# Optimization experiments

Measured on AMD Instinct MI355X. Metric: run time of the kernel, lower is better.

Reference implementation:

```python
import jax, jax.numpy as jnp
import numpy as np

N_NODES = 100000
N_EDGES = 3200000
HID = 128

def lrelu(x):
    return jax.nn.leaky_relu(x, negative_slope=0.01)

def gcn_conv(x, W, b, src, dst):
    # PyG GCNConv: h = x W; add self-loops; sym-normalized scatter-sum; + bias
    N = x.shape[0]
    h = x @ W                                   # [N, out]
    loop = jnp.arange(N, dtype=src.dtype)
    s = jnp.concatenate([src, loop])
    d = jnp.concatenate([dst, loop])
    deg = jnp.zeros((N,), h.dtype).at[d].add(1.0)
    dinv = jnp.where(deg > 0, jax.lax.rsqrt(deg), 0.0)
    norm = dinv[s] * dinv[d]                    # [E+N]
    msgs = h[s] * norm[:, None]                 # gather + scale
    out = jax.ops.segment_sum(msgs, d, num_segments=N)
    return out + b

def setup_inputs() -> dict:
    key = jax.random.key(0)
    ks = jax.random.split(key, 32)
    f = jnp.float32
    def w(k, shape, fan_in):
        return (jax.random.normal(k, shape, dtype=f) * (1.0 / np.sqrt(fan_in))).astype(f)
    inp = {}
    inp['des'] = jax.random.normal(ks[0], (N_NODES, 768), dtype=f)
    inp['tweet'] = jax.random.normal(ks[1], (N_NODES, 768), dtype=f)
    inp['num_prop'] = jax.random.normal(ks[2], (N_NODES, 5), dtype=f)
    inp['cat_prop'] = jax.random.normal(ks[3], (N_NODES, 1), dtype=f)
    inp['edge_index'] = jax.random.randint(ks[4], (2, N_EDGES), 0, N_NODES, dtype=jnp.int32)
    q = HID // 4
    inp['W_des'] = w(ks[5], (768, q), 768);   inp['b_des'] = jnp.zeros((q,), f)
    inp['W_tweet'] = w(ks[6], (768, q), 768); inp['b_tweet'] = jnp.zeros((q,), f)
    inp['W_num'] = w(ks[7], (5, q), 5);       inp['b_num'] = jnp.zeros((q,), f)
    inp['W_cat'] = w(ks[8], (1, q), 1);       inp['b_cat'] = jnp.zeros((q,), f)
    inp['W_in'] = w(ks[9], (HID, HID), HID);  inp['b_in'] = jnp.zeros((HID,), f)
    inp['W_g1'] = w(ks[10], (HID, HID), HID); inp['b_g1'] = jnp.zeros((HID,), f)
    inp['W_g2'] = w(ks[11], (HID, HID), HID); inp['b_g2'] = jnp.zeros((HID,), f)
    inp['W_o1'] = w(ks[12], (HID, HID), HID); inp['b_o1'] = jnp.zeros((HID,), f)
    inp['W_o2'] = w(ks[13], (HID, 2), HID);   inp['b_o2'] = jnp.zeros((2,), f)
    return inp

def reference(des, tweet, num_prop, cat_prop, edge_index,
              W_des, b_des, W_tweet, b_tweet, W_num, b_num, W_cat, b_cat,
              W_in, b_in, W_g1, b_g1, W_g2, b_g2, W_o1, b_o1, W_o2, b_o2):
    src, dst = edge_index[0], edge_index[1]
    d = lrelu(des @ W_des + b_des)
    t = lrelu(tweet @ W_tweet + b_tweet)
    n = lrelu(num_prop @ W_num + b_num)
    c = lrelu(cat_prop @ W_cat + b_cat)
    x = jnp.concatenate((d, t, n, c), axis=1)   # [N, HID]
    x = lrelu(x @ W_in + b_in)                  # dropout = identity (eval)
    x = gcn_conv(x, W_g1, b_g1, src, dst)
    x = gcn_conv(x, W_g2, b_g2, src, dst)
    x = lrelu(x @ W_o1 + b_o1)
    return x @ W_o2 + b_o2                      # [N, 2]
```

## Files before the change

kernel.cpp:

```cpp
#include <hip/hip_runtime.h>
#include <hip/hip_bf16.h>
#include <cstdint>

#define HID 128
#define BSHIFT 11

typedef short short8 __attribute__((ext_vector_type(8)));
typedef float f32x4 __attribute__((ext_vector_type(4)));

__device__ __forceinline__ unsigned pack_bf16(float a, float b)
{
    __hip_bfloat16 ha = __float2bfloat16(a);
    __hip_bfloat16 hb = __float2bfloat16(b);
    unsigned short ua = *reinterpret_cast<unsigned short*>(&ha);
    unsigned short ub = *reinterpret_cast<unsigned short*>(&hb);
    return (unsigned)ua | ((unsigned)ub << 16);
}

__device__ __forceinline__ float bf16_lo(unsigned u)
{
    unsigned v = u << 16;
    return *reinterpret_cast<float*>(&v);
}
__device__ __forceinline__ float bf16_hi(unsigned u)
{
    unsigned v = u & 0xffff0000u;
    return *reinterpret_cast<float*>(&v);
}

__device__ __forceinline__ void split8(const float* v, short8& h, short8& l)
{
    #pragma unroll
    for (int j = 0; j < 8; ++j) {
        unsigned bits = __float_as_uint(v[j]);
        h[j] = (short)(bits >> 16);
        unsigned hb = bits & 0xffff0000u;
        float lof = v[j] - __uint_as_float(hb);
        l[j] = (short)(__float_as_uint(lof) >> 16);
    }
}

__device__ __forceinline__ short8 frag_ld(const short* __restrict__ base, int tile, int lane)
{
    return *reinterpret_cast<const short8*>(base + (((size_t)tile * 64 + lane) << 3));
}

__device__ __forceinline__ int lds_addr(int row, int unit)
{
    return row * 256 + ((unit ^ (row & 7)) << 4);
}

__global__ void convert_w_kernel(
    const float* W0, const float* W1, const float* W2,
    const float* W3, const float* W4, const float* W5,
    short* H0, short* L0, short* H1, short* L1, short* H2, short* L2,
    short* H3, short* L3, short* H4, short* L4, short* H5, short* L5)
{
    int job = blockIdx.y;
    const float* W; short* H; short* L; int K, C;
    switch (job) {
        case 0: W = W0; H = H0; L = L0; K = 768; C = 32;  break;
        case 1: W = W1; H = H1; L = L1; K = 768; C = 32;  break;
        case 2: W = W2; H = H2; L = L2; K = 128; C = 128; break;
        case 3: W = W3; H = H3; L = L3; K = 128; C = 128; break;
        case 4: W = W4; H = H4; L = L4; K = 128; C = 128; break;
        default: W = W5; H = H5; L = L5; K = 128; C = 128; break;
    }
    int NT = C >> 4;
    int rows = (K >> 5) * NT * 64;
    int r = blockIdx.x * blockDim.x + threadIdx.x;
    if (r >= rows) return;
    int lane = r & 63;
    int tile = r >> 6;
    int c = (tile % NT) * 16 + (lane & 15);
    int kbase = (tile / NT) * 32 + ((lane >> 4) & 3) * 8;
    float v[8];
    #pragma unroll
    for (int j = 0; j < 8; ++j) v[j] = W[(size_t)(kbase + j) * C + c];
    short8 h, l;
    split8(v, h, l);
    *reinterpret_cast<short8*>(H + ((size_t)r << 3)) = h;
    *reinterpret_cast<short8*>(L + ((size_t)r << 3)) = l;
}

__global__ __launch_bounds__(256, 4) void enc_lds_kernel(
    const float* __restrict__ des, const float* __restrict__ tweet,
    const short* __restrict__ wdes_hi, const short* __restrict__ wdes_lo,
    const short* __restrict__ wtw_hi, const short* __restrict__ wtw_lo,
    const float* __restrict__ bd, const float* __restrict__ bt,
    float* __restrict__ x0, int N)
{
    __shared__ char lds[2][16384];
    const int mat = blockIdx.y;
    const float* __restrict__ X = mat ? tweet : des;
    const short* __restrict__ WH = mat ? wtw_hi : wdes_hi;
    const short* __restrict__ WL = mat ? wtw_lo : wdes_lo;
    const float* __restrict__ B = mat ? bt : bd;

    const int t = threadIdx.x;
    const int lane = t & 63;
    const int wv = t >> 6;
    const int n0 = blockIdx.x * 64;

    const int srow_in_seg = lane >> 4;
    const int sunit = lane & 15;

    f32x4 acc0 = {}, acc1 = {};

    auto stage = [&](int b, int p) {
        #pragma unroll
        for (int i = 0; i < 4; ++i) {
            int seg = wv * 4 + i;
            int row = seg * 4 + srow_in_seg;
            int qsrc = sunit ^ (row & 7);
            int rowg = n0 + row;
            if (rowg >= N) rowg = N - 1;
            const char* g = (const char*)X + (size_t)rowg * 3072 + (size_t)p * 256 + qsrc * 16;
            __builtin_amdgcn_global_load_lds((const unsigned*)g,
                                             (unsigned*)&lds[b][seg * 1024], 16, 0, 0);
        }
    };

    const int frow = wv * 16 + (lane & 15);
    const int kq = (lane >> 4) * 2;

    stage(0, 0);
    for (int p = 0; p < 12; ++p) {
        const int b = p & 1;
        if (p < 11) stage(b ^ 1, p + 1);
        __syncthreads();
        #pragma unroll
        for (int kcl = 0; kcl < 2; ++kcl) {
            int q0 = kcl * 8 + kq;
            float4 u0 = *reinterpret_cast<const float4*>(
                &lds[b][frow * 256 + ((q0 ^ (frow & 7)) << 4)]);
            float4 u1 = *reinterpret_cast<const float4*>(
                &lds[b][frow * 256 + (((q0 + 1) ^ (frow & 7)) << 4)]);
            float av[8] = {u0.x, u0.y, u0.z, u0.w, u1.x, u1.y, u1.z, u1.w};
            short8 ah, al;
            split8(av, ah, al);
            int kc = p * 2 + kcl;
            short8 wh0 = frag_ld(WH, kc * 2 + 0, lane);
            short8 wl0 = frag_ld(WL, kc * 2 + 0, lane);
            short8 wh1 = frag_ld(WH, kc * 2 + 1, lane);
            short8 wl1 = frag_ld(WL, kc * 2 + 1, lane);
            acc0 = __builtin_amdgcn_mfma_f32_16x16x32_bf16(ah, wh0, acc0, 0, 0, 0);
            acc1 = __builtin_amdgcn_mfma_f32_16x16x32_bf16(ah, wh1, acc1, 0, 0, 0);
            acc0 = __builtin_amdgcn_mfma_f32_16x16x32_bf16(ah, wl0, acc0, 0, 0, 0);
            acc1 = __builtin_amdgcn_mfma_f32_16x16x32_bf16(ah, wl1, acc1, 0, 0, 0);
            acc0 = __builtin_amdgcn_mfma_f32_16x16x32_bf16(al, wh0, acc0, 0, 0, 0);
            acc1 = __builtin_amdgcn_mfma_f32_16x16x32_bf16(al, wh1, acc1, 0, 0, 0);
        }
        __syncthreads();
    }

    const int cl = lane & 15;
    float b0 = B[cl], b1 = B[16 + cl];
    const int nodeb = n0 + wv * 16 + (lane >> 4) * 4;
    #pragma unroll
    for (int r = 0; r < 4; ++r) {
        int node = nodeb + r;
        if (node < N) {
            float v0 = acc0[r] + b0; v0 = v0 > 0.f ? v0 : 0.01f * v0;
            float v1 = acc1[r] + b1; v1 = v1 > 0.f ? v1 : 0.01f * v1;
            x0[(size_t)node * HID + mat * 32 + cl] = v0;
            x0[(size_t)node * HID + mat * 32 + 16 + cl] = v1;
        }
    }
}

__global__ void enc_nc_kernel(const float* __restrict__ num, const float* __restrict__ cat,
                              const float* __restrict__ Wn, const float* __restrict__ bn,
                              const float* __restrict__ Wc, const float* __restrict__ bc,
                              float* __restrict__ x0, int N)
{
    int tid = blockIdx.x * blockDim.x + threadIdx.x;
    int col = tid & 63;
    int node = tid >> 6;
    if (node >= N) return;
    float a;
    if (col < 32) {
        const float* r = num + (size_t)node * 5;
        float acc = bn[col];
        #pragma unroll
        for (int k = 0; k < 5; ++k) acc = fmaf(r[k], Wn[k * 32 + col], acc);
        a = acc;
    } else {
        int c = col & 31;
        a = fmaf(cat[node], Wc[c], bc[c]);
    }
    a = a > 0.f ? a : 0.01f * a;
    x0[(size_t)node * HID + 64 + col] = a;
}

__global__ __launch_bounds__(512, 4) void fused_x1g1_kernel(
    const float* __restrict__ in,
    const short* __restrict__ WH1, const short* __restrict__ WL1, const float* __restrict__ b1,
    const short* __restrict__ WH2, const short* __restrict__ WL2,
    const float* __restrict__ dinv, unsigned* __restrict__ outp, int N)
{
    __shared__ char lds[8 * 4096];
    const int t = threadIdx.x;
    const int lane = t & 63;
    const int wv = t >> 6;
    const int n0 = blockIdx.x * 128;
    const int arow = n0 + wv * 16 + (lane & 15);
    const bool valid = arow < N;
    const int cl = lane & 15;
    const int rq = lane >> 4;

    f32x4 acc[8] = {};
    #pragma unroll
    for (int kc = 0; kc < 4; ++kc) {
        float av[8] = {};
        if (valid) {
            const float* ap = in + (size_t)arow * HID + rq * 8;
            float4 u0 = *reinterpret_cast<const float4*>(ap + kc * 32);
            float4 u1 = *reinterpret_cast<const float4*>(ap + kc * 32 + 4);
            av[0] = u0.x; av[1] = u0.y; av[2] = u0.z; av[3] = u0.w;
            av[4] = u1.x; av[5] = u1.y; av[6] = u1.z; av[7] = u1.w;
        }
        short8 ah, al;
        split8(av, ah, al);
        #pragma unroll
        for (int nt = 0; nt < 8; ++nt) {
            short8 wh = frag_ld(WH1, kc * 8 + nt, lane);
            short8 wl = frag_ld(WL1, kc * 8 + nt, lane);
            acc[nt] = __builtin_amdgcn_mfma_f32_16x16x32_bf16(ah, wh, acc[nt], 0, 0, 0);
            acc[nt] = __builtin_amdgcn_mfma_f32_16x16x32_bf16(ah, wl, acc[nt], 0, 0, 0);
            acc[nt] = __builtin_amdgcn_mfma_f32_16x16x32_bf16(al, wh, acc[nt], 0, 0, 0);
        }
    }

    char* my = lds + wv * 4096;
    #pragma unroll
    for (int nt = 0; nt < 8; ++nt) {
        float bb = b1[nt * 16 + cl];
        #pragma unroll
        for (int r = 0; r < 4; ++r) {
            float v = acc[nt][r] + bb;
            v = v > 0.f ? v : 0.01f * v;
            float pv = __shfl_xor(v, 1);
            if ((lane & 1) == 0) {
                unsigned uv = pack_bf16(v, pv);
                int row = rq * 4 + r;
                int col = nt * 16 + cl;
                int unit = col >> 3;
                int off = ((col & 7) >> 1) << 2;
                *reinterpret_cast<unsigned*>(my + lds_addr(row, unit) + off) = uv;
            }
        }
    }
    __syncthreads();

    f32x4 acc2[8] = {};
    #pragma unroll
    for (int kc = 0; kc < 4; ++kc) {
        short8 ah = *reinterpret_cast<short8*>(my + lds_addr(cl, kc * 4 + rq));
        #pragma unroll
        for (int nt = 0; nt < 8; ++nt) {
            short8 wh = frag_ld(WH2, kc * 8 + nt, lane);
            short8 wl = frag_ld(WL2, kc * 8 + nt, lane);
            acc2[nt] = __builtin_amdgcn_mfma_f32_16x16x32_bf16(ah, wh, acc2[nt], 0, 0, 0);
            acc2[nt] = __builtin_amdgcn_mfma_f32_16x16x32_bf16(ah, wl, acc2[nt], 0, 0, 0);
        }
    }

    const int nodeb = n0 + wv * 16 + rq * 4;
    float di[4];
    #pragma unroll
    for (int r = 0; r < 4; ++r)
        di[r] = (nodeb + r < N) ? dinv[nodeb + r] : 0.f;
    #pragma unroll
    for (int nt = 0; nt < 8; ++nt) {
        int c = nt * 16 + cl;
        #pragma unroll
        for (int r = 0; r < 4; ++r) {
            float v = acc2[nt][r] * di[r];
            float pv = __shfl_xor(v, 1);
            int node = nodeb + r;
            if ((lane & 1) == 0 && node < N) {
                unsigned u = pack_bf16(v, pv);
                outp[(size_t)node * (HID / 2) + (c >> 1)] = u;
            }
        }
    }
}

template<bool OUT2>
__global__ __launch_bounds__(512, 4) void fused_convgemm_kernel(
    const unsigned* __restrict__ hs, const int* __restrict__ row_ptr,
    const int* __restrict__ col_idx, const float* __restrict__ dinv,
    const float* __restrict__ bconv,
    const short* __restrict__ WH, const short* __restrict__ WL,
    const float* __restrict__ bgem, const float* __restrict__ W2,
    const float* __restrict__ b2, void* __restrict__ outp, int N)
{
    __shared__ char lds[32 * 256];
    __shared__ float red[2][16][4][2];
    const int t = threadIdx.x;
    const int lane = t & 63;
    const int wv = t >> 6;
    const int n0 = blockIdx.x * 32;

    {
        int nl = t >> 4;
        int f = t & 15;
        int node = n0 + nl;
        float a[8] = {};
        if (node < N) {
            const uint4* base = reinterpret_cast<const uint4*>(hs);
            uint4 v0 = base[(size_t)node * 16 + f];
            a[0] = bf16_lo(v0.x); a[1] = bf16_hi(v0.x);
            a[2] = bf16_lo(v0.y); a[3] = bf16_hi(v0.y);
            a[4] = bf16_lo(v0.z); a[5] = bf16_hi(v0.z);
            a[6] = bf16_lo(v0.w); a[7] = bf16_hi(v0.w);
            int e = row_ptr[node], end = row_ptr[node + 1];
            int idx = (e + f < end) ? col_idx[e + f] : 0;
            while (e < end) {
                int m = end - e;
                int curidx = idx;
                if (e + 16 + f < end) idx = col_idx[e + 16 + f];
                if (m >= 16) {
                    #pragma unroll 16
                    for (int j = 0; j < 16; ++j) {
                        int s = __shfl(curidx, j, 16);
                        uint4 v = base[(size_t)s * 16 + f];
                        a[0] += bf16_lo(v.x); a[1] += bf16_hi(v.x);
                        a[2] += bf16_lo(v.y); a[3] += bf16_hi(v.y);
                        a[4] += bf16_lo(v.z); a[5] += bf16_hi(v.z);
                        a[6] += bf16_lo(v.w); a[7] += bf16_hi(v.w);
                    }
                    e += 16;
                } else {
                    for (int j = 0; j < m; ++j) {
                        int s = __shfl(curidx, j, 16);
                        uint4 v = base[(size_t)s * 16 + f];
                        a[0] += bf16_lo(v.x); a[1] += bf16_hi(v.x);
                        a[2] += bf16_lo(v.y); a[3] += bf16_hi(v.y);
                        a[4] += bf16_lo(v.z); a[5] += bf16_hi(v.z);
                        a[6] += bf16_lo(v.w); a[7] += bf16_hi(v.w);
                    }
                    e = end;
                }
            }
            float di = dinv[node];
            const float* bb = bconv + f * 8;
            #pragma unroll
            for (int j = 0; j < 8; ++j) a[j] = fmaf(di, a[j], bb[j]);
        }
        uint4 o;
        o.x = pack_bf16(a[0], a[1]);
        o.y = pack_bf16(a[2], a[3]);
        o.z = pack_bf16(a[4], a[5]);
        o.w = pack_bf16(a[6], a[7]);
        *reinterpret_cast<uint4*>(lds + lds_addr(nl, f)) = o;
    }
    __syncthreads();

    const int cl = lane & 15;
    const int rq = lane >> 4;
    const int mt = wv >> 2;
    const int ntp = wv & 3;
    f32x4 acc[2] = {};
    #pragma unroll
    for (int kc = 0; kc < 4; ++kc) {
        short8 ah = *reinterpret_cast<short8*>(lds + lds_addr(mt * 16 + cl, kc * 4 + rq));
        #pragma unroll
        for (int i = 0; i < 2; ++i) {
            int nt = ntp * 2 + i;
            short8 wh = frag_ld(WH, kc * 8 + nt, lane);
            short8 wl = frag_ld(WL, kc * 8 + nt, lane);
            acc[i] = __builtin_amdgcn_mfma_f32_16x16x32_bf16(ah, wh, acc[i], 0, 0, 0);
            acc[i] = __builtin_amdgcn_mfma_f32_16x16x32_bf16(ah, wl, acc[i], 0, 0, 0);
        }
    }

    const int nodeb = n0 + mt * 16 + rq * 4;

    if (!OUT2) {
        float di[4];
        #pragma unroll
        for (int r = 0; r < 4; ++r)
            di[r] = (nodeb + r < N) ? dinv[nodeb + r] : 0.f;
        #pragma unroll
        for (int i = 0; i < 2; ++i) {
            int c = (ntp * 2 + i) * 16 + cl;
            #pragma unroll
            for (int r = 0; r < 4; ++r) {
                float v = acc[i][r] * di[r];
                float pv = __shfl_xor(v, 1);
                int node = nodeb + r;
                if ((lane & 1) == 0 && node < N) {
                    unsigned u = pack_bf16(v, pv);
                    reinterpret_cast<unsigned*>(outp)[(size_t)node * (HID / 2) + (c >> 1)] = u;
                }
            }
        }
    } else {
        float p0[4] = {}, p1[4] = {};
        #pragma unroll
        for (int i = 0; i < 2; ++i) {
            int c = (ntp * 2 + i) * 16 + cl;
            float bb = bgem[c];
            float w20 = W2[c * 2 + 0], w21 = W2[c * 2 + 1];
            #pragma unroll
            for (int r = 0; r < 4; ++r) {
                float v = acc[i][r] + bb;
                v = v > 0.f ? v : 0.01f * v;
                p0[r] = fmaf(v, w20, p0[r]);
                p1[r] = fmaf(v, w21, p1[r]);
            }
        }
        #pragma unroll
        for (int r = 0; r < 4; ++r) {
            #pragma unroll
            for (int m = 1; m < 16; m <<= 1) {
                p0[r] += __shfl_xor(p0[r], m);
                p1[r] += __shfl_xor(p1[r], m);
            }
        }
        if (cl == 0) {
            #pragma unroll
            for (int r = 0; r < 4; ++r) {
                red[mt][rq * 4 + r][ntp][0] = p0[r];
                red[mt][rq * 4 + r][ntp][1] = p1[r];
            }
        }
        __syncthreads();
        if (t < 64) {
            int nl2 = t >> 1, comp = t & 1;
            int mtt = nl2 >> 4, rr = nl2 & 15;
            float s = red[mtt][rr][0][comp] + red[mtt][rr][1][comp]
                    + red[mtt][rr][2][comp] + red[mtt][rr][3][comp] + b2[comp];
            int node = n0 + nl2;
            if (node < N)
                reinterpret_cast<float*>(outp)[(size_t)node * 2 + comp] = s;
        }
    }
}

__global__ void init_gcur_kernel(int* __restrict__ gcur, int NBUCK, int CAP)
{
    int t = threadIdx.x;
    if (t < NBUCK) gcur[t] = t * CAP;
}

__global__ void partition_kernel(const int* __restrict__ src, const int* __restrict__ dst,
                                 int* __restrict__ gcur, int2* __restrict__ pairs,
                                 int E, int maxpos)
{
    __shared__ int sS[1024], sD[1024];
    __shared__ int bcnt[64], boff[64];
    int nch = (E + 1023) >> 10;
    for (int ch = blockIdx.x; ch < nch; ch += gridDim.x) {
        int base = ch << 10;
        int cnt = E - base; if (cnt > 1024) cnt = 1024;
        for (int i = threadIdx.x; i < cnt; i += 256) { sS[i] = src[base + i]; sD[i] = dst[base + i]; }
        if (threadIdx.x < 64) bcnt[threadIdx.x] = 0;
        __syncthreads();
        for (int i = threadIdx.x; i < cnt; i += 256) atomicAdd(&bcnt[sD[i] >> BSHIFT], 1);
        __syncthreads();
        if (threadIdx.x < 64 && bcnt[threadIdx.x] > 0)
            boff[threadIdx.x] = atomicAdd(&gcur[threadIdx.x], bcnt[threadIdx.x]);
        __syncthreads();
        if (threadIdx.x < 64) bcnt[threadIdx.x] = 0;
        __syncthreads();
        for (int i = threadIdx.x; i < cnt; i += 256) {
            int d = sD[i];
            int b = d >> BSHIFT;
            int r = atomicAdd(&bcnt[b], 1);
            int pos = boff[b] + r;
            if (pos < maxpos) pairs[pos] = make_int2(sS[i], d);
        }
        __syncthreads();
    }
}

__global__ void hist_bucket_kernel(const int2* __restrict__ pairs, const int* __restrict__ gcur,
                                   int* __restrict__ cnt, int CAP, int N)
{
    __shared__ int lc[2048];
    int b = blockIdx.x;
    int half = blockIdx.y;
    int beg = b * CAP;
    int size = gcur[b] - beg;
    for (int i = threadIdx.x; i < 2048; i += 256) lc[i] = 0;
    __syncthreads();
    int s0 = beg + half * (size >> 1);
    int s1 = half ? (beg + size) : (beg + (size >> 1));
    for (int i = s0 + threadIdx.x; i < s1; i += 256)
        atomicAdd(&lc[pairs[i].y & 2047], 1);
    __syncthreads();
    int nodeb = b << BSHIFT;
    for (int i = threadIdx.x; i < 2048; i += 256) {
        if (lc[i] && nodeb + i < N) atomicAdd(&cnt[nodeb + i], lc[i]);
    }
}

__global__ void scan_block_kernel(const int* __restrict__ cnt, int* __restrict__ excl_out,
                                  int* __restrict__ part, int N)
{
    __shared__ int s[256];
    int t = threadIdx.x;
    int i = blockIdx.x * 256 + t;
    int v = (i < N) ? cnt[i] : 0;
    s[t] = v;
    __syncthreads();
    #pragma unroll
    for (int off = 1; off < 256; off <<= 1) {
        int x = (t >= off) ? s[t - off] : 0;
        __syncthreads();
        s[t] += x;
        __syncthreads();
    }
    int incl = s[t];
    if (i < N) excl_out[i] = incl - v;
    if (t == 255) part[blockIdx.x] = incl;
}

__global__ void scan_part_kernel(int* __restrict__ part, int B)
{
    __shared__ int s[512];
    int t = threadIdx.x;
    int v = (t < B) ? part[t] : 0;
    s[t] = v;
    __syncthreads();
    #pragma unroll
    for (int off = 1; off < 512; off <<= 1) {
        int x = (t >= off) ? s[t - off] : 0;
        __syncthreads();
        s[t] += x;
        __syncthreads();
    }
    int incl = s[t];
    if (t < B) part[t] = incl - v;
    if (t == B - 1) part[B] = incl;
}

__global__ void scan_final_kernel(int* __restrict__ row_ptr, const int* __restrict__ part,
                                  int* __restrict__ cursor, const int* __restrict__ cnt,
                                  float* __restrict__ dinv, int N, int B)
{
    int i = blockIdx.x * blockDim.x + threadIdx.x;
    if (i < N) {
        int rp = row_ptr[i] + part[i >> 8];
        row_ptr[i] = rp;
        cursor[i] = rp;
        dinv[i] = rsqrtf((float)(cnt[i] + 1));
    } else if (i == N) {
        row_ptr[N] = part[B];
    }
}

__global__ void scatterB_kernel(const int2* __restrict__ pairs, const int* __restrict__ gcur,
                                int* __restrict__ cursor, int* __restrict__ col_idx, int CAP)
{
    int b = blockIdx.x >> 2;
    int q = blockIdx.x & 3;
    int beg = b * CAP;
    int size = gcur[b] - beg;
    int qs = beg + (int)(((long long)size * q) >> 2);
    int qe = beg + (int)(((long long)size * (q + 1)) >> 2);
    for (int i = qs + threadIdx.x; i < qe; i += 256) {
        int2 p = pairs[i];
        int pos = atomicAdd(&cursor[p.y], 1);
        col_idx[pos] = p.x;
    }
}

extern "C" void kernel_launch(void* const* d_in, const int* in_sizes, int n_in,
                              void* d_out, int out_size, void* d_ws, size_t ws_size,
                              hipStream_t stream)
{
    const float* des   = (const float*)d_in[0];
    const float* tweet = (const float*)d_in[1];
    const float* num   = (const float*)d_in[2];
    const float* cat   = (const float*)d_in[3];
    const int*   eidx  = (const int*)d_in[4];
    const float* W_des = (const float*)d_in[5];  const float* b_des = (const float*)d_in[6];
    const float* W_tw  = (const float*)d_in[7];  const float* b_tw  = (const float*)d_in[8];
    const float* W_num = (const float*)d_in[9];  const float* b_num = (const float*)d_in[10];
    const float* W_cat = (const float*)d_in[11]; const float* b_cat = (const float*)d_in[12];
    const float* W_in  = (const float*)d_in[13]; const float* b_in  = (const float*)d_in[14];
    const float* W_g1  = (const float*)d_in[15]; const float* b_g1  = (const float*)d_in[16];
    const float* W_g2  = (const float*)d_in[17]; const float* b_g2  = (const float*)d_in[18];
    const float* W_o1  = (const float*)d_in[19]; const float* b_o1  = (const float*)d_in[20];
    const float* W_o2  = (const float*)d_in[21]; const float* b_o2  = (const float*)d_in[22];
    float* out = (float*)d_out;

    const int N = in_sizes[0] / 768;
    const int E = in_sizes[4] / 2;
    const int* src = eidx;
    const int* dst = eidx + E;

    const int NBUCK = (N + 2047) >> BSHIFT;
    const int CAP = (E / (NBUCK > 0 ? NBUCK : 1)) + (E / (NBUCK > 0 ? NBUCK : 1)) / 4 + 4096;

    char* ws = (char*)d_ws;
    const size_t szF = (size_t)N * HID * sizeof(float);
    float* F0 = (float*)ws;                    ws += szF;
    float* F1 = (float*)ws;                    ws += szF;
    float* F2 = (float*)ws;                    ws += szF;
    int* cnt      = (int*)ws;                  ws += ((size_t)N * 4 + 255) & ~255ULL;
    int* row_ptr  = (int*)ws;                  ws += (((size_t)N + 1) * 4 + 255) & ~255ULL;
    int* cursor   = (int*)ws;                  ws += ((size_t)N * 4 + 255) & ~255ULL;
    int* part     = (int*)ws;                  ws += 4096;
    float* dinv   = (float*)ws;                ws += ((size_t)N * 4 + 255) & ~255ULL;
    int* gcur     = (int*)ws;                  ws += 256;
    const size_t sz768 = 768 * 32 * sizeof(short);
    const size_t sz128 = 128 * 128 * sizeof(short);
    short* wdes_hi = (short*)ws; ws += sz768;  short* wdes_lo = (short*)ws; ws += sz768;
    short* wtw_hi  = (short*)ws; ws += sz768;  short* wtw_lo  = (short*)ws; ws += sz768;
    short* win_hi  = (short*)ws; ws += sz128;  short* win_lo  = (short*)ws; ws += sz128;
    short* wg1_hi  = (short*)ws; ws += sz128;  short* wg1_lo  = (short*)ws; ws += sz128;
    short* wg2_hi  = (short*)ws; ws += sz128;  short* wg2_lo  = (short*)ws; ws += sz128;
    short* wo1_hi  = (short*)ws; ws += sz128;  short* wo1_lo  = (short*)ws; ws += sz128;
    int* col_idx  = (int*)ws;                  ws += ((size_t)E * 4 + 255) & ~255ULL;
    int2* pairs   = (int2*)ws;                 ws += (size_t)NBUCK * CAP * 8;

    const int B = (N + 255) / 256;

    {
        dim3 grid(12, 6);
        convert_w_kernel<<<grid, 256, 0, stream>>>(
            W_des, W_tw, W_in, W_g1, W_g2, W_o1,
            wdes_hi, wdes_lo, wtw_hi, wtw_lo, win_hi, win_lo,
            wg1_hi, wg1_lo, wg2_hi, wg2_lo, wo1_hi, wo1_lo);
    }

    hipMemsetAsync(cnt, 0, (size_t)N * sizeof(int), stream);
    init_gcur_kernel<<<1, 64, 0, stream>>>(gcur, NBUCK, CAP);
    partition_kernel<<<1024, 256, 0, stream>>>(src, dst, gcur, pairs, E, NBUCK * CAP);
    {
        dim3 hg(NBUCK, 2);
        hist_bucket_kernel<<<hg, 256, 0, stream>>>(pairs, gcur, cnt, CAP, N);
    }
    scan_block_kernel<<<B, 256, 0, stream>>>(cnt, row_ptr, part, N);
    scan_part_kernel<<<1, 512, 0, stream>>>(part, B);
    scan_final_kernel<<<(N + 256) / 256 + 1, 256, 0, stream>>>(row_ptr, part, cursor, cnt, dinv, N, B);
    scatterB_kernel<<<NBUCK * 4, 256, 0, stream>>>(pairs, gcur, cursor, col_idx, CAP);

    {
        dim3 grid((N + 63) / 64, 2);
        enc_lds_kernel<<<grid, 256, 0, stream>>>(des, tweet, wdes_hi, wdes_lo,
                                                 wtw_hi, wtw_lo, b_des, b_tw, F0, N);
        enc_nc_kernel<<<((size_t)N * 64 + 255) / 256, 256, 0, stream>>>(num, cat, W_num, b_num, W_cat, b_cat, F0, N);
    }

    fused_x1g1_kernel<<<(N + 127) / 128, 512, 0, stream>>>(
        F0, win_hi, win_lo, b_in, wg1_hi, wg1_lo, dinv, (unsigned*)F2, N);

    fused_convgemm_kernel<false><<<(N + 31) / 32, 512, 0, stream>>>(
        (const unsigned*)F2, row_ptr, col_idx, dinv, b_g1,
        wg2_hi, wg2_lo, nullptr, nullptr, nullptr, F1, N);

    fused_convgemm_kernel<true><<<(N + 31) / 32, 512, 0, stream>>>(
        (const unsigned*)F1, row_ptr, col_idx, dinv, b_g2,
        wo1_hi, wo1_lo, b_o1, W_o2, b_o2, out, N);
}
```

Measured before the change: 732.7 us.

## Merge encoder GEMM, edge partition and small-feature encoder into one heterogeneous launch

Combines the dense des/tweet encoder, the edge bucket partition and the num/cat encoder into a single kernel whose blocks branch by index range. The bandwidth-heavy encoder and the atomic-heavy partition can then run concurrently, and two launches plus the gcur init kernel go away. gcur now holds per-bucket offsets starting at zero and is cleared with a memset. The histogram and scatter kernels now split each bucket four and eight ways. Risks: the partition loses its maxpos overflow guard, and blocks with different resource use now share one launch.

```diff
diff --git a/kernel.cpp b/kernel.cpp
--- a/kernel.cpp
+++ b/kernel.cpp
@@ -83,15 +83,14 @@
     *reinterpret_cast<short8*>(L + ((size_t)r << 3)) = l;
 }
 
-__global__ __launch_bounds__(256, 4) void enc_lds_kernel(
-    const float* __restrict__ des, const float* __restrict__ tweet,
-    const short* __restrict__ wdes_hi, const short* __restrict__ wdes_lo,
-    const short* __restrict__ wtw_hi, const short* __restrict__ wtw_lo,
-    const float* __restrict__ bd, const float* __restrict__ bt,
-    float* __restrict__ x0, int N)
-{
-    __shared__ char lds[2][16384];
-    const int mat = blockIdx.y;
+__device__ void enc_body(char* smem, int xb, int mat,
+                         const float* __restrict__ des, const float* __restrict__ tweet,
+                         const short* __restrict__ wdes_hi, const short* __restrict__ wdes_lo,
+                         const short* __restrict__ wtw_hi, const short* __restrict__ wtw_lo,
+                         const float* __restrict__ bd, const float* __restrict__ bt,
+                         float* __restrict__ x0, int N)
+{
+    char (*lds)[16384] = reinterpret_cast<char(*)[16384]>(smem);
     const float* __restrict__ X = mat ? tweet : des;
     const short* __restrict__ WH = mat ? wtw_hi : wdes_hi;
     const short* __restrict__ WL = mat ? wtw_lo : wdes_lo;
@@ -100,7 +99,7 @@
     const int t = threadIdx.x;
     const int lane = t & 63;
     const int wv = t >> 6;
-    const int n0 = blockIdx.x * 64;
+    const int n0 = xb * 64;
 
     const int srow_in_seg = lane >> 4;
     const int sunit = lane & 15;
@@ -169,28 +168,178 @@
     }
 }
 
-__global__ void enc_nc_kernel(const float* __restrict__ num, const float* __restrict__ cat,
-                              const float* __restrict__ Wn, const float* __restrict__ bn,
-                              const float* __restrict__ Wc, const float* __restrict__ bc,
-                              float* __restrict__ x0, int N)
-{
-    int tid = blockIdx.x * blockDim.x + threadIdx.x;
-    int col = tid & 63;
-    int node = tid >> 6;
-    if (node >= N) return;
-    float a;
-    if (col < 32) {
-        const float* r = num + (size_t)node * 5;
-        float acc = bn[col];
-        #pragma unroll
-        for (int k = 0; k < 5; ++k) acc = fmaf(r[k], Wn[k * 32 + col], acc);
-        a = acc;
+__device__ void partition_body(char* smem, int pb, int partB,
+                               const int* __restrict__ src, const int* __restrict__ dst,
+                               int* __restrict__ gcur, int2* __restrict__ pairs,
+                               int E, int CAP)
+{
+    int* sS = reinterpret_cast<int*>(smem);
+    int* sD = sS + 1024;
+    int* bcnt = sD + 1024;
+    int* boff = bcnt + 64;
+    int nch = (E + 1023) >> 10;
+    for (int ch = pb; ch < nch; ch += partB) {
+        int base = ch << 10;
+        int cnt = E - base; if (cnt > 1024) cnt = 1024;
+        for (int i = threadIdx.x; i < cnt; i += 256) { sS[i] = src[base + i]; sD[i] = dst[base + i]; }
+        if (threadIdx.x < 64) bcnt[threadIdx.x] = 0;
+        __syncthreads();
+        for (int i = threadIdx.x; i < cnt; i += 256) atomicAdd(&bcnt[sD[i] >> BSHIFT], 1);
+        __syncthreads();
+        if (threadIdx.x < 64 && bcnt[threadIdx.x] > 0)
+            boff[threadIdx.x] = atomicAdd(&gcur[threadIdx.x], bcnt[threadIdx.x]);
+        __syncthreads();
+        if (threadIdx.x < 64) bcnt[threadIdx.x] = 0;
+        __syncthreads();
+        for (int i = threadIdx.x; i < cnt; i += 256) {
+            int d = sD[i];
+            int b = d >> BSHIFT;
+            int r = atomicAdd(&bcnt[b], 1);
+            int pos = b * CAP + boff[b] + r;
+            pairs[pos] = make_int2(sS[i], d);
+        }
+        __syncthreads();
+    }
+}
+
+__device__ void encnc_body(int nb, int ncB,
+                           const float* __restrict__ num, const float* __restrict__ cat,
+                           const float* __restrict__ Wn, const float* __restrict__ bn,
+                           const float* __restrict__ Wc, const float* __restrict__ bc,
+                           float* __restrict__ x0, int N)
+{
+    long long total = (long long)N * 64;
+    for (long long i = (long long)nb * 256 + threadIdx.x; i < total; i += (long long)ncB * 256) {
+        int col = (int)(i & 63);
+        int node = (int)(i >> 6);
+        float a;
+        if (col < 32) {
+            const float* r = num + (size_t)node * 5;
+            float acc = bn[col];
+            #pragma unroll
+            for (int k = 0; k < 5; ++k) acc = fmaf(r[k], Wn[k * 32 + col], acc);
+            a = acc;
+        } else {
+            int c = col & 31;
+            a = fmaf(cat[node], Wc[c], bc[c]);
+        }
+        a = a > 0.f ? a : 0.01f * a;
+        x0[(size_t)node * HID + 64 + col] = a;
+    }
+}
+
+__global__ __launch_bounds__(256, 4) void mega_kernel(
+    const float* des, const float* tweet,
+    const short* wdes_hi, const short* wdes_lo,
+    const short* wtw_hi, const short* wtw_lo,
+    const float* bd, const float* bt, float* x0,
+    const int* src, const int* dst, int* gcur, int2* pairs, int E, int CAP,
+    const float* num, const float* cat,
+    const float* Wn, const float* bn, const float* Wc, const float* bc,
+    int N, int encB, int partB, int ncB)
+{
+    __shared__ char smem[32768];
+    int b = blockIdx.x;
+    if (b < encB) {
+        enc_body(smem, b >> 1, b & 1, des, tweet, wdes_hi, wdes_lo,
+                 wtw_hi, wtw_lo, bd, bt, x0, N);
+    } else if (b < encB + partB) {
+        partition_body(smem, b - encB, partB, src, dst, gcur, pairs, E, CAP);
     } else {
-        int c = col & 31;
-        a = fmaf(cat[node], Wc[c], bc[c]);
-    }
-    a = a > 0.f ? a : 0.01f * a;
-    x0[(size_t)node * HID + 64 + col] = a;
+        encnc_body(b - encB - partB, ncB, num, cat, Wn, bn, Wc, bc, x0, N);
+    }
+}
+
+__global__ void hist_bucket_kernel(const int2* __restrict__ pairs, const int* __restrict__ gcur,
+                                   int* __restrict__ cnt, int CAP, int N)
+{
+    __shared__ int lc[2048];
+    int b = blockIdx.x;
+    int q = blockIdx.y;
+    int beg = b * CAP;
+    int size = gcur[b];
+    for (int i = threadIdx.x; i < 2048; i += 256) lc[i] = 0;
+    __syncthreads();
+    int s0 = beg + (int)(((long long)size * q) >> 2);
+    int s1 = beg + (int)(((long long)size * (q + 1)) >> 2);
+    for (int i = s0 + threadIdx.x; i < s1; i += 256)
+        atomicAdd(&lc[pairs[i].y & 2047], 1);
+    __syncthreads();
+    int nodeb = b << BSHIFT;
+    for (int i = threadIdx.x; i < 2048; i += 256) {
+        if (lc[i] && nodeb + i < N) atomicAdd(&cnt[nodeb + i], lc[i]);
+    }
+}
+
+__global__ void scan_block_kernel(const int* __restrict__ cnt, int* __restrict__ excl_out,
+                                  int* __restrict__ part, int N)
+{
+    __shared__ int s[256];
+    int t = threadIdx.x;
+    int i = blockIdx.x * 256 + t;
+    int v = (i < N) ? cnt[i] : 0;
+    s[t] = v;
+    __syncthreads();
+    #pragma unroll
+    for (int off = 1; off < 256; off <<= 1) {
+        int x = (t >= off) ? s[t - off] : 0;
+        __syncthreads();
+        s[t] += x;
+        __syncthreads();
+    }
+    int incl = s[t];
+    if (i < N) excl_out[i] = incl - v;
+    if (t == 255) part[blockIdx.x] = incl;
+}
+
+__global__ void scan_part_kernel(int* __restrict__ part, int B)
+{
+    __shared__ int s[512];
+    int t = threadIdx.x;
+    int v = (t < B) ? part[t] : 0;
+    s[t] = v;
+    __syncthreads();
+    #pragma unroll
+    for (int off = 1; off < 512; off <<= 1) {
+        int x = (t >= off) ? s[t - off] : 0;
+        __syncthreads();
+        s[t] += x;
+        __syncthreads();
+    }
+    int incl = s[t];
+    if (t < B) part[t] = incl - v;
+    if (t == B - 1) part[B] = incl;
+}
+
+__global__ void scan_final_kernel(int* __restrict__ row_ptr, const int* __restrict__ part,
+                                  int* __restrict__ cursor, const int* __restrict__ cnt,
+                                  float* __restrict__ dinv, int N, int B)
+{
+    int i = blockIdx.x * blockDim.x + threadIdx.x;
+    if (i < N) {
+        int rp = row_ptr[i] + part[i >> 8];
+        row_ptr[i] = rp;
+        cursor[i] = rp;
+        dinv[i] = rsqrtf((float)(cnt[i] + 1));
+    } else if (i == N) {
+        row_ptr[N] = part[B];
+    }
+}
+
+__global__ void scatterB_kernel(const int2* __restrict__ pairs, const int* __restrict__ gcur,
+                                int* __restrict__ cursor, int* __restrict__ col_idx, int CAP)
+{
+    int b = blockIdx.x >> 3;
+    int q = blockIdx.x & 7;
+    int beg = b * CAP;
+    int size = gcur[b];
+    int qs = beg + (int)(((long long)size * q) >> 3);
+    int qe = beg + (int)(((long long)size * (q + 1)) >> 3);
+    for (int i = qs + threadIdx.x; i < qe; i += 256) {
+        int2 p = pairs[i];
+        int pos = atomicAdd(&cursor[p.y], 1);
+        col_idx[pos] = p.x;
+    }
 }
 
 __global__ __launch_bounds__(512, 4) void fused_x1g1_kernel(
@@ -440,135 +589,6 @@
     }
 }
 
-__global__ void init_gcur_kernel(int* __restrict__ gcur, int NBUCK, int CAP)
-{
-    int t = threadIdx.x;
-    if (t < NBUCK) gcur[t] = t * CAP;
-}
-
-__global__ void partition_kernel(const int* __restrict__ src, const int* __restrict__ dst,
-                                 int* __restrict__ gcur, int2* __restrict__ pairs,
-                                 int E, int maxpos)
-{
-    __shared__ int sS[1024], sD[1024];
-    __shared__ int bcnt[64], boff[64];
-    int nch = (E + 1023) >> 10;
-    for (int ch = blockIdx.x; ch < nch; ch += gridDim.x) {
-        int base = ch << 10;
-        int cnt = E - base; if (cnt > 1024) cnt = 1024;
-        for (int i = threadIdx.x; i < cnt; i += 256) { sS[i] = src[base + i]; sD[i] = dst[base + i]; }
-        if (threadIdx.x < 64) bcnt[threadIdx.x] = 0;
-        __syncthreads();
-        for (int i = threadIdx.x; i < cnt; i += 256) atomicAdd(&bcnt[sD[i] >> BSHIFT], 1);
-        __syncthreads();
-        if (threadIdx.x < 64 && bcnt[threadIdx.x] > 0)
-            boff[threadIdx.x] = atomicAdd(&gcur[threadIdx.x], bcnt[threadIdx.x]);
-        __syncthreads();
-        if (threadIdx.x < 64) bcnt[threadIdx.x] = 0;
-        __syncthreads();
-        for (int i = threadIdx.x; i < cnt; i += 256) {
-            int d = sD[i];
-            int b = d >> BSHIFT;
-            int r = atomicAdd(&bcnt[b], 1);
-            int pos = boff[b] + r;
-            if (pos < maxpos) pairs[pos] = make_int2(sS[i], d);
-        }
-        __syncthreads();
-    }
-}
-
-__global__ void hist_bucket_kernel(const int2* __restrict__ pairs, const int* __restrict__ gcur,
-                                   int* __restrict__ cnt, int CAP, int N)
-{
-    __shared__ int lc[2048];
-    int b = blockIdx.x;
-    int half = blockIdx.y;
-    int beg = b * CAP;
-    int size = gcur[b] - beg;
-    for (int i = threadIdx.x; i < 2048; i += 256) lc[i] = 0;
-    __syncthreads();
-    int s0 = beg + half * (size >> 1);
-    int s1 = half ? (beg + size) : (beg + (size >> 1));
-    for (int i = s0 + threadIdx.x; i < s1; i += 256)
-        atomicAdd(&lc[pairs[i].y & 2047], 1);
-    __syncthreads();
-    int nodeb = b << BSHIFT;
-    for (int i = threadIdx.x; i < 2048; i += 256) {
-        if (lc[i] && nodeb + i < N) atomicAdd(&cnt[nodeb + i], lc[i]);
-    }
-}
-
-__global__ void scan_block_kernel(const int* __restrict__ cnt, int* __restrict__ excl_out,
-                                  int* __restrict__ part, int N)
-{
-    __shared__ int s[256];
-    int t = threadIdx.x;
-    int i = blockIdx.x * 256 + t;
-    int v = (i < N) ? cnt[i] : 0;
-    s[t] = v;
-    __syncthreads();
-    #pragma unroll
-    for (int off = 1; off < 256; off <<= 1) {
-        int x = (t >= off) ? s[t - off] : 0;
-        __syncthreads();
-        s[t] += x;
-        __syncthreads();
-    }
-    int incl = s[t];
-    if (i < N) excl_out[i] = incl - v;
-    if (t == 255) part[blockIdx.x] = incl;
-}
-
-__global__ void scan_part_kernel(int* __restrict__ part, int B)
-{
-    __shared__ int s[512];
-    int t = threadIdx.x;
-    int v = (t < B) ? part[t] : 0;
-    s[t] = v;
-    __syncthreads();
-    #pragma unroll
-    for (int off = 1; off < 512; off <<= 1) {
-        int x = (t >= off) ? s[t - off] : 0;
-        __syncthreads();
-        s[t] += x;
-        __syncthreads();
-    }
-    int incl = s[t];
-    if (t < B) part[t] = incl - v;
-    if (t == B - 1) part[B] = incl;
-}
-
-__global__ void scan_final_kernel(int* __restrict__ row_ptr, const int* __restrict__ part,
-                                  int* __restrict__ cursor, const int* __restrict__ cnt,
-                                  float* __restrict__ dinv, int N, int B)
-{
-    int i = blockIdx.x * blockDim.x + threadIdx.x;
-    if (i < N) {
-        int rp = row_ptr[i] + part[i >> 8];
-        row_ptr[i] = rp;
-        cursor[i] = rp;
-        dinv[i] = rsqrtf((float)(cnt[i] + 1));
-    } else if (i == N) {
-        row_ptr[N] = part[B];
-    }
-}
-
-__global__ void scatterB_kernel(const int2* __restrict__ pairs, const int* __restrict__ gcur,
-                                int* __restrict__ cursor, int* __restrict__ col_idx, int CAP)
-{
-    int b = blockIdx.x >> 2;
-    int q = blockIdx.x & 3;
-    int beg = b * CAP;
-    int size = gcur[b] - beg;
-    int qs = beg + (int)(((long long)size * q) >> 2);
-    int qe = beg + (int)(((long long)size * (q + 1)) >> 2);
-    for (int i = qs + threadIdx.x; i < qe; i += 256) {
-        int2 p = pairs[i];
-        int pos = atomicAdd(&cursor[p.y], 1);
-        col_idx[pos] = p.x;
-    }
-}
-
 extern "C" void kernel_launch(void* const* d_in, const int* in_sizes, int n_in,
                               void* d_out, int out_size, void* d_ws, size_t ws_size,
                               hipStream_t stream)
@@ -629,24 +649,28 @@
             wg1_hi, wg1_lo, wg2_hi, wg2_lo, wo1_hi, wo1_lo);
     }
 
+    hipMemsetAsync(gcur, 0, 256, stream);
     hipMemsetAsync(cnt, 0, (size_t)N * sizeof(int), stream);
-    init_gcur_kernel<<<1, 64, 0, stream>>>(gcur, NBUCK, CAP);
-    partition_kernel<<<1024, 256, 0, stream>>>(src, dst, gcur, pairs, E, NBUCK * CAP);
+
     {
-        dim3 hg(NBUCK, 2);
+        int encB = ((N + 63) / 64) * 2;
+        int partB = 1024;
+        int ncB = 2048;
+        mega_kernel<<<encB + partB + ncB, 256, 0, stream>>>(
+            des, tweet, wdes_hi, wdes_lo, wtw_hi, wtw_lo, b_des, b_tw, F0,
+            src, dst, gcur, pairs, E, CAP,
+            num, cat, W_num, b_num, W_cat, b_cat,
+            N, encB, partB, ncB);
+    }
+
+    {
+        dim3 hg(NBUCK, 4);
         hist_bucket_kernel<<<hg, 256, 0, stream>>>(pairs, gcur, cnt, CAP, N);
     }
     scan_block_kernel<<<B, 256, 0, stream>>>(cnt, row_ptr, part, N);
     scan_part_kernel<<<1, 512, 0, stream>>>(part, B);
     scan_final_kernel<<<(N + 256) / 256 + 1, 256, 0, stream>>>(row_ptr, part, cursor, cnt, dinv, N, B);
-    scatterB_kernel<<<NBUCK * 4, 256, 0, stream>>>(pairs, gcur, cursor, col_idx, CAP);
-
-    {
-        dim3 grid((N + 63) / 64, 2);
-        enc_lds_kernel<<<grid, 256, 0, stream>>>(des, tweet, wdes_hi, wdes_lo,
-                                                 wtw_hi, wtw_lo, b_des, b_tw, F0, N);
-        enc_nc_kernel<<<((size_t)N * 64 + 255) / 256, 256, 0, stream>>>(num, cat, W_num, b_num, W_cat, b_cat, F0, N);
-    }
+    scatterB_kernel<<<NBUCK * 8, 256, 0, stream>>>(pairs, gcur, cursor, col_idx, CAP);
 
     fused_x1g1_kernel<<<(N + 127) / 128, 512, 0, stream>>>(
         F0, win_hi, win_lo, b_in, wg1_hi, wg1_lo, dinv, (unsigned*)F2, N);
```

Measured after the change: 750.2 us. 1.02x slower.
